# Performance work log

Measured on AMD Instinct MI355X. Metric: run time of the kernel, lower is better.

## Reference

```python
import jax, jax.numpy as jnp
import numpy as np

N_NODES = 50000
N_EDGES = 800000
IN_DIM = 128
HIDDEN = 32
HEADS = 4
OUT_DIM = 64
NEG_SLOPE = 0.2  # PyG GATConv default


def setup_inputs() -> dict:
    key = jax.random.key(0)
    ks = jax.random.split(key, 12)
    s = 0.05
    return {
        "x": jax.random.normal(ks[0], (N_NODES, IN_DIM), dtype=jnp.float32),
        "edge_index": jax.random.randint(ks[1], (2, N_EDGES), 0, N_NODES, dtype=jnp.int64),
        # layer 1: out = HEADS * HIDDEN, concat=True
        "W1": jax.random.normal(ks[2], (IN_DIM, HEADS * HIDDEN), dtype=jnp.float32) * s,
        "a_src1": jax.random.normal(ks[3], (HEADS, HIDDEN), dtype=jnp.float32) * s,
        "a_dst1": jax.random.normal(ks[4], (HEADS, HIDDEN), dtype=jnp.float32) * s,
        "b1": jnp.zeros((HEADS * HIDDEN,), dtype=jnp.float32),
        # layer 2: heads=1, concat=False
        "W2": jax.random.normal(ks[5], (HEADS * HIDDEN, OUT_DIM), dtype=jnp.float32) * s,
        "a_src2": jax.random.normal(ks[6], (1, OUT_DIM), dtype=jnp.float32) * s,
        "a_dst2": jax.random.normal(ks[7], (1, OUT_DIM), dtype=jnp.float32) * s,
        "b2": jnp.zeros((OUT_DIM,), dtype=jnp.float32),
    }


def _gat_conv(x, src, dst, W, a_src, a_dst, b, heads, concat):
    """PyG-style GATConv. src/dst already include self-loops."""
    N = x.shape[0]
    C = W.shape[1] // heads
    h = (x @ W).reshape(N, heads, C)              # [N,H,C]
    al_s = jnp.sum(h * a_src, axis=-1)            # [N,H]
    al_d = jnp.sum(h * a_dst, axis=-1)            # [N,H]
    e = jax.nn.leaky_relu(al_s[src] + al_d[dst], NEG_SLOPE)  # [E,H]
    # numerically-stable segment softmax over incoming edges of each dst node
    m = jax.ops.segment_max(e, dst, num_segments=N)          # [N,H]
    ex = jnp.exp(e - m[dst])
    denom = jax.ops.segment_sum(ex, dst, num_segments=N)     # [N,H]
    alpha = ex / denom[dst]                                   # [E,H]
    out = jax.ops.segment_sum(h[src] * alpha[:, :, None], dst, num_segments=N)  # [N,H,C]
    out = out.reshape(N, heads * C) if concat else out.mean(axis=1)
    return out + b


def reference(x, edge_index, W1, a_src1, a_dst1, b1, W2, a_src2, a_dst2, b2):
    N = x.shape[0]
    loop = jnp.arange(N, dtype=edge_index.dtype)
    src = jnp.concatenate([edge_index[0], loop])
    dst = jnp.concatenate([edge_index[1], loop])
    h = jax.nn.relu(_gat_conv(x, src, dst, W1, a_src1, a_dst1, b1, HEADS, True))
    out = _gat_conv(h, src, dst, W2, a_src2, a_dst2, b2, 1, False)
    return jax.nn.log_softmax(out, axis=1)
```

## Files before the change

kernel.cpp:

```cpp
#include <hip/hip_runtime.h>
#include <hip/hip_bf16.h>
#include <math.h>

#define N_NODES 50000
#define N_EDGES 800000
#define E_TOT   (N_EDGES + N_NODES)
#define IN_DIM  128
#define HID     128
#define ODIM    64
#define NEG     0.2f
#define NB1     ((N_NODES + 255) / 256)
#define NCHUNK  ((N_NODES + 31) / 32)
#define NREP    8
#define MM1B    512
#define EGRID   ((E_TOT + 255) / 256)

typedef short bf16x8 __attribute__((ext_vector_type(8)));
typedef float f32x4 __attribute__((ext_vector_type(4)));
typedef float f32x2 __attribute__((ext_vector_type(2)));
typedef unsigned short ushort_t;

__device__ __forceinline__ float lrelu(float x) { return x >= 0.f ? x : NEG * x; }

__device__ __forceinline__ unsigned short f2b(float v) {
  unsigned int b = __float_as_uint(v);
  b += 0x7fffu + ((b >> 16) & 1u);
  return (unsigned short)(b >> 16);
}
__device__ __forceinline__ unsigned int f2b2(float lo, float hi) {
  union { __hip_bfloat162 h; unsigned int u; } cv;
  cv.h = __float22bfloat162_rn(make_float2(lo, hi));
  return cv.u;
}
__device__ __forceinline__ f32x2 f8x2lo(unsigned int v) {
  return __builtin_amdgcn_cvt_pk_f32_fp8((int)v, false);
}
__device__ __forceinline__ f32x2 f8x2hi(unsigned int v) {
  return __builtin_amdgcn_cvt_pk_f32_fp8((int)v, true);
}
__device__ __forceinline__ unsigned char f2f8(float v) {
  return (unsigned char)(__builtin_amdgcn_cvt_pk_fp8_f32(v, v, 0, false) & 0xff);
}

__device__ __forceinline__ int e_src(const void* ei, int f, int e) {
  if (e >= N_EDGES) return e - N_EDGES;
  return f ? (int)((const long long*)ei)[e] : ((const int*)ei)[e];
}
__device__ __forceinline__ int e_dst(const void* ei, int f, int e) {
  if (e >= N_EDGES) return e - N_EDGES;
  return f ? (int)((const long long*)ei)[N_EDGES + e] : ((const int*)ei)[N_EDGES + e];
}

__global__ void k_prep(const float* __restrict__ W1, const float* __restrict__ W2,
                       ushort_t* __restrict__ Wt1, ushort_t* __restrict__ Wt2,
                       const void* ei, int* flag, int4* __restrict__ degr4) {
  if (blockIdx.x == 64) {
    if (threadIdx.x == 0) {
      const int* p = (const int*)ei;
      int allz = 1;
      for (int i = 0; i < 64; ++i) if (p[2 * i + 1] != 0) { allz = 0; break; }
      *flag = allz;
    }
    return;
  }
  if (blockIdx.x > 64) {
    int i = (blockIdx.x - 65) * 256 + threadIdx.x;
    if (i < NREP * N_NODES / 4) degr4[i] = make_int4(0, 0, 0, 0);
    return;
  }
  int i = blockIdx.x * 256 + threadIdx.x;
  if (i < 128 * 128) { int k = i >> 7, n = i & 127; Wt1[n * 128 + k] = f2b(W1[i]); }
  if (i < 128 * 64)  { int k = i >> 6, n = i & 63;  Wt2[n * 128 + k] = f2b(W2[i]); }
}

__global__ void k_scan1(const int* __restrict__ degr, int* __restrict__ offs, int* __restrict__ bsums) {
  __shared__ int sm[256];
  int t = threadIdx.x, i = blockIdx.x * 256 + t;
  int v = 0;
  if (i < N_NODES) {
    #pragma unroll
    for (int r = 0; r < NREP; ++r) v += degr[r * N_NODES + i];
  }
  sm[t] = v;
  __syncthreads();
  for (int o = 1; o < 256; o <<= 1) {
    int add = (t >= o) ? sm[t - o] : 0;
    __syncthreads();
    sm[t] += add;
    __syncthreads();
  }
  if (i < N_NODES) offs[i] = sm[t] - v;
  if (t == 255) bsums[blockIdx.x] = sm[255];
}

__global__ void k_scan3(int* __restrict__ offs, const int* __restrict__ bsums,
                        const int* __restrict__ degr, int* __restrict__ repbase) {
  __shared__ int red[4];
  int t = threadIdx.x;
  int v = (t < blockIdx.x) ? bsums[t] : 0;
  #pragma unroll
  for (int o = 32; o >= 1; o >>= 1) v += __shfl_xor(v, o);
  if ((t & 63) == 0) red[t >> 6] = v;
  __syncthreads();
  int pre = red[0] + red[1] + red[2] + red[3];
  int i = blockIdx.x * 256 + t;
  if (i < N_NODES) {
    int o = offs[i] + pre;
    offs[i] = o;
    int run = o;
    #pragma unroll
    for (int r = 0; r < NREP; ++r) {
      repbase[r * N_NODES + i] = run;
      run += degr[r * N_NODES + i];
    }
  }
  if (i == 0) offs[N_NODES] = E_TOT;
}

__global__ void k_scatter(const void* ei, const int* __restrict__ flag,
                          const int* __restrict__ repbase,
                          const int* __restrict__ rank, int* __restrict__ srcs) {
  int e = blockIdx.x * 256 + threadIdx.x;
  if (e >= E_TOT) return;
  int f = *flag;
  int d = e_dst(ei, f, e);
  int r = blockIdx.x & (NREP - 1);
  srcs[repbase[r * N_NODES + d] + rank[e]] = e_src(ei, f, e);
}

__global__ __launch_bounds__(256) void k_mm1h(const float* __restrict__ x,
                                              const ushort_t* __restrict__ Wt,
                                              unsigned char* __restrict__ h1f8,
                                              float* __restrict__ als1,
                                              float* __restrict__ ald1,
                                              const float* __restrict__ asrc,
                                              const float* __restrict__ adst,
                                              const void* ei, const int* __restrict__ flag,
                                              int* __restrict__ degr, int* __restrict__ rank) {
  if (blockIdx.x >= MM1B) {
    int e = (blockIdx.x - MM1B) * 256 + threadIdx.x;
    if (e < E_TOT) {
      int r = (blockIdx.x - MM1B) & (NREP - 1);
      int d = e_dst(ei, *flag, e);
      rank[e] = atomicAdd(&degr[r * N_NODES + d], 1);
    }
    return;
  }
  __shared__ ushort_t xs[32 * 128];
  int t = threadIdx.x;
  int w = t >> 6, l = t & 63;
  int lr = l & 15, lk = l >> 4;
  int nodeSub = (w & 1) * 16, colBase = (w >> 1) * 64;
  int headBase = colBase >> 5;
  bf16x8 bfrag[4][4];
  #pragma unroll
  for (int ct = 0; ct < 4; ++ct)
    #pragma unroll
    for (int ks = 0; ks < 4; ++ks) {
      int n = colBase + ct * 16 + lr;
      int k = ks * 32 + lk * 8;
      bfrag[ct][ks] = *(const bf16x8*)&Wt[n * 128 + k];
    }
  float as0 = asrc[colBase + lr],      as1v = asrc[colBase + 16 + lr];
  float as2 = asrc[colBase + 32 + lr], as3 = asrc[colBase + 48 + lr];
  float ad0 = adst[colBase + lr],      ad1v = adst[colBase + 16 + lr];
  float ad2 = adst[colBase + 32 + lr], ad3 = adst[colBase + 48 + lr];
  int rr = t >> 3, c0 = (t & 7) * 16;
  for (int chunk = blockIdx.x; chunk < NCHUNK; chunk += MM1B) {
    int base = chunk * 32;
    int srcRow = base + rr; if (srcRow >= N_NODES) srcRow = N_NODES - 1;
    const float4* xr = (const float4*)&x[(size_t)srcRow * IN_DIM + c0];
    float4 f0 = xr[0], f1 = xr[1], f2 = xr[2], f3 = xr[3];
    uint4 w0, w1;
    w0.x = f2b2(f0.x, f0.y); w0.y = f2b2(f0.z, f0.w);
    w0.z = f2b2(f1.x, f1.y); w0.w = f2b2(f1.z, f1.w);
    w1.x = f2b2(f2.x, f2.y); w1.y = f2b2(f2.z, f2.w);
    w1.z = f2b2(f3.x, f3.y); w1.w = f2b2(f3.z, f3.w);
    char* xsb = (char*)xs;
    int swz = (rr & 7) << 4;
    *(uint4*)(xsb + rr * 256 + ((c0 * 2 +  0) ^ swz)) = w0;
    *(uint4*)(xsb + rr * 256 + ((c0 * 2 + 16) ^ swz)) = w1;
    __syncthreads();
    f32x4 acc[4] = {{0,0,0,0},{0,0,0,0},{0,0,0,0},{0,0,0,0}};
    int arow = nodeSub + lr;
    #pragma unroll
    for (int ks = 0; ks < 4; ++ks) {
      bf16x8 a = *(const bf16x8*)((const char*)xs + arow * 256 +
                                  ((ks * 64 + lk * 16) ^ ((arow & 7) << 4)));
      #pragma unroll
      for (int ct = 0; ct < 4; ++ct)
        acc[ct] = __builtin_amdgcn_mfma_f32_16x16x32_bf16(a, bfrag[ct][ks], acc[ct], 0, 0, 0);
    }
    __syncthreads();
    #pragma unroll
    for (int r = 0; r < 4; ++r) {
      int node = base + nodeSub + lk * 4 + r;
      if (node < N_NODES) {
        h1f8[(size_t)node * HID + colBase +      lr] = f2f8(acc[0][r]);
        h1f8[(size_t)node * HID + colBase + 16 + lr] = f2f8(acc[1][r]);
        h1f8[(size_t)node * HID + colBase + 32 + lr] = f2f8(acc[2][r]);
        h1f8[(size_t)node * HID + colBase + 48 + lr] = f2f8(acc[3][r]);
      }
      float s01 = acc[0][r] * as0 + acc[1][r] * as1v;
      float s23 = acc[2][r] * as2 + acc[3][r] * as3;
      float d01 = acc[0][r] * ad0 + acc[1][r] * ad1v;
      float d23 = acc[2][r] * ad2 + acc[3][r] * ad3;
      #pragma unroll
      for (int o = 1; o <= 8; o <<= 1) {
        s01 += __shfl_xor(s01, o); s23 += __shfl_xor(s23, o);
        d01 += __shfl_xor(d01, o); d23 += __shfl_xor(d23, o);
      }
      if (lr == 0 && node < N_NODES) {
        als1[node * 4 + headBase]     = s01;
        als1[node * 4 + headBase + 1] = s23;
        ald1[node * 4 + headBase]     = d01;
        ald1[node * 4 + headBase + 1] = d23;
      }
    }
  }
}

__global__ __launch_bounds__(256) void k_mm2(const ushort_t* __restrict__ xb,
                                             const ushort_t* __restrict__ Wt,
                                             unsigned char* __restrict__ h2f8,
                                             float* __restrict__ als2,
                                             float* __restrict__ ald2,
                                             const float* __restrict__ asrc,
                                             const float* __restrict__ adst) {
  __shared__ ushort_t xs[32 * 128];
  __shared__ float als_lds[32], ald_lds[32];
  int t = threadIdx.x;
  int w = t >> 6, l = t & 63;
  int lr = l & 15, lk = l >> 4;
  int nodeSub = (w & 1) * 16, colBase = (w >> 1) * 32;
  bf16x8 bfrag[2][4];
  #pragma unroll
  for (int ct = 0; ct < 2; ++ct)
    #pragma unroll
    for (int ks = 0; ks < 4; ++ks) {
      int n = colBase + ct * 16 + lr;
      int k = ks * 32 + lk * 8;
      bfrag[ct][ks] = *(const bf16x8*)&Wt[n * 128 + k];
    }
  float as0 = asrc[colBase + lr], as1v = asrc[colBase + 16 + lr];
  float ad0 = adst[colBase + lr], ad1v = adst[colBase + 16 + lr];
  int rr = t >> 3, c0 = (t & 7) * 16;
  for (int chunk = blockIdx.x; chunk < NCHUNK; chunk += gridDim.x) {
    int base = chunk * 32;
    int srcRow = base + rr; if (srcRow >= N_NODES) srcRow = N_NODES - 1;
    const uint4* xr = (const uint4*)&xb[(size_t)srcRow * HID + c0];
    uint4 w0 = xr[0], w1 = xr[1];
    char* xsb = (char*)xs;
    int swz = (rr & 7) << 4;
    *(uint4*)(xsb + rr * 256 + ((c0 * 2 +  0) ^ swz)) = w0;
    *(uint4*)(xsb + rr * 256 + ((c0 * 2 + 16) ^ swz)) = w1;
    __syncthreads();
    f32x4 acc[2] = {{0,0,0,0},{0,0,0,0}};
    int arow = nodeSub + lr;
    #pragma unroll
    for (int ks = 0; ks < 4; ++ks) {
      bf16x8 a = *(const bf16x8*)((const char*)xs + arow * 256 +
                                  ((ks * 64 + lk * 16) ^ ((arow & 7) << 4)));
      #pragma unroll
      for (int ct = 0; ct < 2; ++ct)
        acc[ct] = __builtin_amdgcn_mfma_f32_16x16x32_bf16(a, bfrag[ct][ks], acc[ct], 0, 0, 0);
    }
    if (t < 32) { als_lds[t] = 0.f; ald_lds[t] = 0.f; }
    __syncthreads();
    #pragma unroll
    for (int r = 0; r < 4; ++r) {
      int nodeLocal = nodeSub + lk * 4 + r;
      int node = base + nodeLocal;
      if (node < N_NODES) {
        h2f8[(size_t)node * ODIM + colBase +      lr] = f2f8(acc[0][r]);
        h2f8[(size_t)node * ODIM + colBase + 16 + lr] = f2f8(acc[1][r]);
      }
      float s = acc[0][r] * as0 + acc[1][r] * as1v;
      float d = acc[0][r] * ad0 + acc[1][r] * ad1v;
      #pragma unroll
      for (int o = 1; o <= 8; o <<= 1) {
        s += __shfl_xor(s, o);
        d += __shfl_xor(d, o);
      }
      if (lr == 0) {
        atomicAdd(&als_lds[nodeLocal], s);
        atomicAdd(&ald_lds[nodeLocal], d);
      }
    }
    __syncthreads();
    if (t < 32) {
      int node = base + t;
      if (node < N_NODES) { als2[node] = als_lds[t]; ald2[node] = ald_lds[t]; }
    }
  }
}

__global__ __launch_bounds__(256) void k_agg1(const unsigned char* __restrict__ h1f8,
                                              const float* __restrict__ als,
                                              const float* __restrict__ ald, const int* __restrict__ offs,
                                              const int* __restrict__ srcs, const float* __restrict__ b1,
                                              ushort_t* __restrict__ out1b) {
  int t = threadIdx.x;
  int w = t >> 6, l = t & 63;
  int hw = l >> 5, lh = l & 31;
  int sg = lh >> 4, cl = lh & 15, head = cl >> 2;
  int n = blockIdx.x * 8 + w * 2 + hw;
  int off0 = offs[n], deg = offs[n + 1] - off0;
  float adh = ald[n * 4 + head];
  const unsigned char* hb = h1f8 + cl * 8;

  float ds = 0.f;
  float num0 = 0, num1 = 0, num2 = 0, num3 = 0, num4 = 0, num5 = 0, num6 = 0, num7 = 0;

  int j = sg;
  for (; j + 2 < deg; j += 4) {
    int sA = srcs[off0 + j];
    int sB = srcs[off0 + j + 2];
    float aA = als[sA * 4 + head];
    float aB = als[sB * 4 + head];
    uint2 vA = *(const uint2*)(hb + (sA << 7));
    uint2 vB = *(const uint2*)(hb + (sB << 7));
    float wA = __expf(lrelu(aA + adh));
    float wB = __expf(lrelu(aB + adh));
    ds += wA + wB;
    f32x2 p0 = f8x2lo(vA.x), p1 = f8x2hi(vA.x);
    f32x2 p2 = f8x2lo(vA.y), p3 = f8x2hi(vA.y);
    num0 = fmaf(wA, p0.x, num0); num1 = fmaf(wA, p0.y, num1);
    num2 = fmaf(wA, p1.x, num2); num3 = fmaf(wA, p1.y, num3);
    num4 = fmaf(wA, p2.x, num4); num5 = fmaf(wA, p2.y, num5);
    num6 = fmaf(wA, p3.x, num6); num7 = fmaf(wA, p3.y, num7);
    p0 = f8x2lo(vB.x); p1 = f8x2hi(vB.x);
    p2 = f8x2lo(vB.y); p3 = f8x2hi(vB.y);
    num0 = fmaf(wB, p0.x, num0); num1 = fmaf(wB, p0.y, num1);
    num2 = fmaf(wB, p1.x, num2); num3 = fmaf(wB, p1.y, num3);
    num4 = fmaf(wB, p2.x, num4); num5 = fmaf(wB, p2.y, num5);
    num6 = fmaf(wB, p3.x, num6); num7 = fmaf(wB, p3.y, num7);
  }
  if (j < deg) {
    int sA = srcs[off0 + j];
    float aA = als[sA * 4 + head];
    uint2 vA = *(const uint2*)(hb + (sA << 7));
    float wA = __expf(lrelu(aA + adh));
    ds += wA;
    f32x2 p0 = f8x2lo(vA.x), p1 = f8x2hi(vA.x);
    f32x2 p2 = f8x2lo(vA.y), p3 = f8x2hi(vA.y);
    num0 = fmaf(wA, p0.x, num0); num1 = fmaf(wA, p0.y, num1);
    num2 = fmaf(wA, p1.x, num2); num3 = fmaf(wA, p1.y, num3);
    num4 = fmaf(wA, p2.x, num4); num5 = fmaf(wA, p2.y, num5);
    num6 = fmaf(wA, p3.x, num6); num7 = fmaf(wA, p3.y, num7);
  }
  num0 += __shfl_xor(num0, 16); num1 += __shfl_xor(num1, 16);
  num2 += __shfl_xor(num2, 16); num3 += __shfl_xor(num3, 16);
  num4 += __shfl_xor(num4, 16); num5 += __shfl_xor(num5, 16);
  num6 += __shfl_xor(num6, 16); num7 += __shfl_xor(num7, 16);
  ds += __shfl_xor(ds, 16);
  if (lh < 16) {
    float rd = 1.f / ds;
    int c8 = cl * 8;
    float4 bb0 = *(const float4*)&b1[c8];
    float4 bb1 = *(const float4*)&b1[c8 + 4];
    float o0 = fmaxf(num0 * rd + bb0.x, 0.f);
    float o1 = fmaxf(num1 * rd + bb0.y, 0.f);
    float o2 = fmaxf(num2 * rd + bb0.z, 0.f);
    float o3 = fmaxf(num3 * rd + bb0.w, 0.f);
    float o4 = fmaxf(num4 * rd + bb1.x, 0.f);
    float o5 = fmaxf(num5 * rd + bb1.y, 0.f);
    float o6 = fmaxf(num6 * rd + bb1.z, 0.f);
    float o7 = fmaxf(num7 * rd + bb1.w, 0.f);
    uint4 pk;
    pk.x = f2b2(o0, o1); pk.y = f2b2(o2, o3);
    pk.z = f2b2(o4, o5); pk.w = f2b2(o6, o7);
    *(uint4*)&out1b[(size_t)n * HID + c8] = pk;
  }
}

__global__ __launch_bounds__(256) void k_agg2(const unsigned char* __restrict__ h2f8,
                                              const float* __restrict__ als,
                                              const float* __restrict__ ald, const int* __restrict__ offs,
                                              const int* __restrict__ srcs, const float* __restrict__ b2,
                                              float* __restrict__ out) {
  int t = threadIdx.x;
  int w = t >> 6, l = t & 63;
  int hw = l >> 5, lh = l & 31;
  int sg = lh >> 3, cl = lh & 7;
  int n = blockIdx.x * 8 + w * 2 + hw;
  int off0 = offs[n], deg = offs[n + 1] - off0;
  float adv = ald[n];
  const unsigned char* hb = h2f8 + cl * 8;

  float ds = 0.f;
  float num0 = 0, num1 = 0, num2 = 0, num3 = 0, num4 = 0, num5 = 0, num6 = 0, num7 = 0;

  int j = sg;
  for (; j + 4 < deg; j += 8) {
    int sA = srcs[off0 + j];
    int sB = srcs[off0 + j + 4];
    float aA = als[sA];
    float aB = als[sB];
    uint2 vA = *(const uint2*)(hb + (sA << 6));
    uint2 vB = *(const uint2*)(hb + (sB << 6));
    float wA = __expf(lrelu(aA + adv));
    float wB = __expf(lrelu(aB + adv));
    ds += wA + wB;
    f32x2 p0 = f8x2lo(vA.x), p1 = f8x2hi(vA.x);
    f32x2 p2 = f8x2lo(vA.y), p3 = f8x2hi(vA.y);
    num0 = fmaf(wA, p0.x, num0); num1 = fmaf(wA, p0.y, num1);
    num2 = fmaf(wA, p1.x, num2); num3 = fmaf(wA, p1.y, num3);
    num4 = fmaf(wA, p2.x, num4); num5 = fmaf(wA, p2.y, num5);
    num6 = fmaf(wA, p3.x, num6); num7 = fmaf(wA, p3.y, num7);
    p0 = f8x2lo(vB.x); p1 = f8x2hi(vB.x);
    p2 = f8x2lo(vB.y); p3 = f8x2hi(vB.y);
    num0 = fmaf(wB, p0.x, num0); num1 = fmaf(wB, p0.y, num1);
    num2 = fmaf(wB, p1.x, num2); num3 = fmaf(wB, p1.y, num3);
    num4 = fmaf(wB, p2.x, num4); num5 = fmaf(wB, p2.y, num5);
    num6 = fmaf(wB, p3.x, num6); num7 = fmaf(wB, p3.y, num7);
  }
  if (j < deg) {
    int sA = srcs[off0 + j];
    float aA = als[sA];
    uint2 vA = *(const uint2*)(hb + (sA << 6));
    float wA = __expf(lrelu(aA + adv));
    ds += wA;
    f32x2 p0 = f8x2lo(vA.x), p1 = f8x2hi(vA.x);
    f32x2 p2 = f8x2lo(vA.y), p3 = f8x2hi(vA.y);
    num0 = fmaf(wA, p0.x, num0); num1 = fmaf(wA, p0.y, num1);
    num2 = fmaf(wA, p1.x, num2); num3 = fmaf(wA, p1.y, num3);
    num4 = fmaf(wA, p2.x, num4); num5 = fmaf(wA, p2.y, num5);
    num6 = fmaf(wA, p3.x, num6); num7 = fmaf(wA, p3.y, num7);
  }
  #pragma unroll
  for (int o = 8; o <= 16; o <<= 1) {
    num0 += __shfl_xor(num0, o); num1 += __shfl_xor(num1, o);
    num2 += __shfl_xor(num2, o); num3 += __shfl_xor(num3, o);
    num4 += __shfl_xor(num4, o); num5 += __shfl_xor(num5, o);
    num6 += __shfl_xor(num6, o); num7 += __shfl_xor(num7, o);
    ds += __shfl_xor(ds, o);
  }
  if (lh < 8) {
    float rd = 1.f / ds;
    int c8 = cl * 8;
    float4 bb0 = *(const float4*)&b2[c8];
    float4 bb1 = *(const float4*)&b2[c8 + 4];
    float v0 = num0 * rd + bb0.x, v1 = num1 * rd + bb0.y;
    float v2 = num2 * rd + bb0.z, v3 = num3 * rd + bb0.w;
    float v4 = num4 * rd + bb1.x, v5 = num5 * rd + bb1.y;
    float v6 = num6 * rd + bb1.z, v7 = num7 * rd + bb1.w;
    float mx = fmaxf(fmaxf(fmaxf(v0, v1), fmaxf(v2, v3)), fmaxf(fmaxf(v4, v5), fmaxf(v6, v7)));
    #pragma unroll
    for (int o = 1; o <= 4; o <<= 1) mx = fmaxf(mx, __shfl_xor(mx, o));
    float sum = __expf(v0 - mx) + __expf(v1 - mx) + __expf(v2 - mx) + __expf(v3 - mx)
              + __expf(v4 - mx) + __expf(v5 - mx) + __expf(v6 - mx) + __expf(v7 - mx);
    #pragma unroll
    for (int o = 1; o <= 4; o <<= 1) sum += __shfl_xor(sum, o);
    float ls = __logf(sum);
    float4 r0, r1;
    r0.x = (v0 - mx) - ls; r0.y = (v1 - mx) - ls; r0.z = (v2 - mx) - ls; r0.w = (v3 - mx) - ls;
    r1.x = (v4 - mx) - ls; r1.y = (v5 - mx) - ls; r1.z = (v6 - mx) - ls; r1.w = (v7 - mx) - ls;
    *(float4*)&out[(size_t)n * ODIM + c8] = r0;
    *(float4*)&out[(size_t)n * ODIM + c8 + 4] = r1;
  }
}

extern "C" void kernel_launch(void* const* d_in, const int* in_sizes, int n_in,
                              void* d_out, int out_size, void* d_ws, size_t ws_size,
                              hipStream_t stream) {
  const float* x   = (const float*)d_in[0];
  const void*  ei  = d_in[1];
  const float* W1  = (const float*)d_in[2];
  const float* as1 = (const float*)d_in[3];
  const float* ad1 = (const float*)d_in[4];
  const float* b1  = (const float*)d_in[5];
  const float* W2  = (const float*)d_in[6];
  const float* as2 = (const float*)d_in[7];
  const float* ad2 = (const float*)d_in[8];
  const float* b2  = (const float*)d_in[9];
  float* out = (float*)d_out;

  char* ws = (char*)d_ws;
  size_t o = 0;
  auto alloc = [&](size_t bytes) { void* p = (void*)(ws + o); o += (bytes + 255) & ~(size_t)255; return p; };
  ushort_t* out1b = (ushort_t*)alloc((size_t)N_NODES * HID * 2);
  unsigned char* h1f8 = (unsigned char*)alloc((size_t)N_NODES * HID);
  ushort_t* Wt1   = (ushort_t*)alloc((size_t)128 * 128 * 2);
  ushort_t* Wt2   = (ushort_t*)alloc((size_t)64 * 128 * 2);
  float* als1 = (float*)alloc((size_t)N_NODES * 4 * 4);
  float* ald1 = (float*)alloc((size_t)N_NODES * 4 * 4);
  float* als2 = (float*)alloc((size_t)N_NODES * 4);
  float* ald2 = (float*)alloc((size_t)N_NODES * 4);
  int*   degr = (int*)alloc((size_t)NREP * N_NODES * 4);
  int*   repbase = (int*)alloc((size_t)NREP * N_NODES * 4);
  int*   offs = (int*)alloc((size_t)(N_NODES + 1) * 4);
  int*   rank = (int*)alloc((size_t)E_TOT * 4);
  int*   srcs = (int*)alloc((size_t)E_TOT * 4);
  int*   bsums= (int*)alloc((size_t)NB1 * 4);
  int*   flag = (int*)alloc(4);
  unsigned char* h2f8 = (unsigned char*)rank;

  int prepGrid = 65 + (NREP * N_NODES / 4 + 255) / 256;
  k_prep   <<<prepGrid, 256, 0, stream>>>(W1, W2, Wt1, Wt2, ei, flag, (int4*)degr);

  k_mm1h   <<<MM1B + EGRID, 256, 0, stream>>>(x, Wt1, h1f8, als1, ald1, as1, ad1,
                                              ei, flag, degr, rank);
  k_scan1  <<<NB1, 256, 0, stream>>>(degr, offs, bsums);
  k_scan3  <<<NB1, 256, 0, stream>>>(offs, bsums, degr, repbase);
  k_scatter<<<EGRID, 256, 0, stream>>>(ei, flag, repbase, rank, srcs);

  k_agg1 <<<N_NODES / 8, 256, 0, stream>>>(h1f8, als1, ald1, offs, srcs, b1, out1b);

  k_mm2  <<<512, 256, 0, stream>>>(out1b, Wt2, h2f8, als2, ald2, as2, ad2);
  k_agg2 <<<N_NODES / 8, 256, 0, stream>>>(h2f8, als2, ald2, offs, srcs, b2, out);
}
```

Baseline: 120.0 us.

## Fuse two-pass scan via grid-wide counter, cache int32 dst, raise replica count

Merges the two scan kernels into one that publishes block sums and spins on a global counter, removing a kernel launch and the round-trip re-read of offsets. The edge-counting pass now stores each edge's destination as int32 so the scatter does not re-decode the edge index. Atomic replica count is doubled to cut contention on degree counters, at the cost of more zeroing and scan reads. The spin barrier assumes all 196 blocks are co-resident, which holds on this GPU but is not guaranteed in general.

```diff
diff --git a/kernel.cpp b/kernel.cpp
--- a/kernel.cpp
+++ b/kernel.cpp
@@ -11,7 +11,7 @@
 #define NEG     0.2f
 #define NB1     ((N_NODES + 255) / 256)
 #define NCHUNK  ((N_NODES + 31) / 32)
-#define NREP    8
+#define NREP    16
 #define MM1B    512
 #define EGRID   ((E_TOT + 255) / 256)
 
@@ -53,7 +53,8 @@
 
 __global__ void k_prep(const float* __restrict__ W1, const float* __restrict__ W2,
                        ushort_t* __restrict__ Wt1, ushort_t* __restrict__ Wt2,
-                       const void* ei, int* flag, int4* __restrict__ degr4) {
+                       const void* ei, int* flag, int4* __restrict__ degr4,
+                       int* __restrict__ ctr) {
   if (blockIdx.x == 64) {
     if (threadIdx.x == 0) {
       const int* p = (const int*)ei;
@@ -61,6 +62,7 @@
       for (int i = 0; i < 64; ++i) if (p[2 * i + 1] != 0) { allz = 0; break; }
       *flag = allz;
     }
+    if (threadIdx.x == 1) *ctr = 0;
     return;
   }
   if (blockIdx.x > 64) {
@@ -73,9 +75,13 @@
   if (i < 128 * 64)  { int k = i >> 6, n = i & 63;  Wt2[n * 128 + k] = f2b(W2[i]); }
 }
 
-__global__ void k_scan1(const int* __restrict__ degr, int* __restrict__ offs, int* __restrict__ bsums) {
+__global__ __launch_bounds__(256) void k_scan(const int* __restrict__ degr, int* __restrict__ offs,
+                                              int* __restrict__ repbase, int* __restrict__ bsums,
+                                              int* __restrict__ ctr) {
   __shared__ int sm[256];
-  int t = threadIdx.x, i = blockIdx.x * 256 + t;
+  __shared__ int red[4];
+  int t = threadIdx.x, b = blockIdx.x;
+  int i = b * 256 + t;
   int v = 0;
   if (i < N_NODES) {
     #pragma unroll
@@ -89,23 +95,24 @@
     sm[t] += add;
     __syncthreads();
   }
-  if (i < N_NODES) offs[i] = sm[t] - v;
-  if (t == 255) bsums[blockIdx.x] = sm[255];
-}
-
-__global__ void k_scan3(int* __restrict__ offs, const int* __restrict__ bsums,
-                        const int* __restrict__ degr, int* __restrict__ repbase) {
-  __shared__ int red[4];
-  int t = threadIdx.x;
-  int v = (t < blockIdx.x) ? bsums[t] : 0;
+  int lexcl = sm[t] - v;
+  if (t == 255) {
+    __hip_atomic_store(&bsums[b], sm[255], __ATOMIC_RELEASE, __HIP_MEMORY_SCOPE_AGENT);
+    __threadfence();
+    atomicAdd(ctr, 1);
+  }
+  if (t == 0) {
+    while (__hip_atomic_load(ctr, __ATOMIC_ACQUIRE, __HIP_MEMORY_SCOPE_AGENT) < (int)gridDim.x) {}
+  }
+  __syncthreads();
+  int p = (t < b) ? __hip_atomic_load(&bsums[t], __ATOMIC_ACQUIRE, __HIP_MEMORY_SCOPE_AGENT) : 0;
   #pragma unroll
-  for (int o = 32; o >= 1; o >>= 1) v += __shfl_xor(v, o);
-  if ((t & 63) == 0) red[t >> 6] = v;
+  for (int o = 32; o >= 1; o >>= 1) p += __shfl_xor(p, o);
+  if ((t & 63) == 0) red[t >> 6] = p;
   __syncthreads();
   int pre = red[0] + red[1] + red[2] + red[3];
-  int i = blockIdx.x * 256 + t;
   if (i < N_NODES) {
-    int o = offs[i] + pre;
+    int o = lexcl + pre;
     offs[i] = o;
     int run = o;
     #pragma unroll
@@ -118,14 +125,13 @@
 }
 
 __global__ void k_scatter(const void* ei, const int* __restrict__ flag,
-                          const int* __restrict__ repbase,
-                          const int* __restrict__ rank, int* __restrict__ srcs) {
+                          const int* __restrict__ repbase, const int* __restrict__ rank,
+                          const int* __restrict__ dst32, int* __restrict__ srcs) {
   int e = blockIdx.x * 256 + threadIdx.x;
   if (e >= E_TOT) return;
-  int f = *flag;
-  int d = e_dst(ei, f, e);
+  int d = dst32[e];
   int r = blockIdx.x & (NREP - 1);
-  srcs[repbase[r * N_NODES + d] + rank[e]] = e_src(ei, f, e);
+  srcs[repbase[r * N_NODES + d] + rank[e]] = e_src(ei, *flag, e);
 }
 
 __global__ __launch_bounds__(256) void k_mm1h(const float* __restrict__ x,
@@ -136,13 +142,15 @@
                                               const float* __restrict__ asrc,
                                               const float* __restrict__ adst,
                                               const void* ei, const int* __restrict__ flag,
-                                              int* __restrict__ degr, int* __restrict__ rank) {
+                                              int* __restrict__ degr, int* __restrict__ rank,
+                                              int* __restrict__ dst32) {
   if (blockIdx.x >= MM1B) {
     int e = (blockIdx.x - MM1B) * 256 + threadIdx.x;
     if (e < E_TOT) {
       int r = (blockIdx.x - MM1B) & (NREP - 1);
       int d = e_dst(ei, *flag, e);
       rank[e] = atomicAdd(&degr[r * N_NODES + d], 1);
+      dst32[e] = d;
     }
     return;
   }
@@ -491,19 +499,20 @@
   int*   repbase = (int*)alloc((size_t)NREP * N_NODES * 4);
   int*   offs = (int*)alloc((size_t)(N_NODES + 1) * 4);
   int*   rank = (int*)alloc((size_t)E_TOT * 4);
+  int*   dst32 = (int*)alloc((size_t)E_TOT * 4);
   int*   srcs = (int*)alloc((size_t)E_TOT * 4);
   int*   bsums= (int*)alloc((size_t)NB1 * 4);
   int*   flag = (int*)alloc(4);
+  int*   ctr  = (int*)alloc(4);
   unsigned char* h2f8 = (unsigned char*)rank;
 
   int prepGrid = 65 + (NREP * N_NODES / 4 + 255) / 256;
-  k_prep   <<<prepGrid, 256, 0, stream>>>(W1, W2, Wt1, Wt2, ei, flag, (int4*)degr);
+  k_prep   <<<prepGrid, 256, 0, stream>>>(W1, W2, Wt1, Wt2, ei, flag, (int4*)degr, ctr);
 
   k_mm1h   <<<MM1B + EGRID, 256, 0, stream>>>(x, Wt1, h1f8, als1, ald1, as1, ad1,
-                                              ei, flag, degr, rank);
-  k_scan1  <<<NB1, 256, 0, stream>>>(degr, offs, bsums);
-  k_scan3  <<<NB1, 256, 0, stream>>>(offs, bsums, degr, repbase);
-  k_scatter<<<EGRID, 256, 0, stream>>>(ei, flag, repbase, rank, srcs);
+                                              ei, flag, degr, rank, dst32);
+  k_scan   <<<NB1, 256, 0, stream>>>(degr, offs, repbase, bsums, ctr);
+  k_scatter<<<EGRID, 256, 0, stream>>>(ei, flag, repbase, rank, dst32, srcs);
 
   k_agg1 <<<N_NODES / 8, 256, 0, stream>>>(h1f8, als1, ald1, offs, srcs, b1, out1b);
 
```

Result: slower. 137.9 us (+14.8%).
